# Kernel tuning notes

Measured on AMD Instinct MI355X. Metric: run time of the kernel, lower is better.

## Reference

```python
import jax, jax.numpy as jnp
import numpy as np

NUM_HEADS = 8

def setup_inputs() -> dict:
    key = jax.random.key(0)
    ks = jax.random.split(key, 10)
    B, S, D = 4, 2048, 512
    scale = 1.0 / np.sqrt(D)
    return {
        "x": jax.random.normal(ks[0], (B, S, D), dtype=jnp.float32),
        "q": jax.random.normal(ks[1], (B, S, D), dtype=jnp.float32),
        "Wq": jax.random.normal(ks[2], (D, D), dtype=jnp.float32) * scale,
        "bq": jax.random.normal(ks[3], (D,), dtype=jnp.float32) * 0.01,
        "Wk": jax.random.normal(ks[4], (D, D), dtype=jnp.float32) * scale,
        "bk": jax.random.normal(ks[5], (D,), dtype=jnp.float32) * 0.01,
        "Wv": jax.random.normal(ks[6], (D, D), dtype=jnp.float32) * scale,
        "bv": jax.random.normal(ks[7], (D,), dtype=jnp.float32) * 0.01,
        "Wo": jax.random.normal(ks[8], (D, D), dtype=jnp.float32) * scale,
        "bo": jax.random.normal(ks[9], (D,), dtype=jnp.float32) * 0.01,
    }

def reference(x, q, Wq, bq, Wk, bk, Wv, bv, Wo, bo):
    B, S, D = x.shape
    H = NUM_HEADS
    Dh = D // H
    # Linear layers: y = x @ W.T + b (torch nn.Linear convention)
    def split_heads(t):  # [B,S,D] -> [B,H,S,Dh]
        return t.reshape(B, -1, H, Dh).transpose(0, 2, 1, 3)
    Q = split_heads(q @ Wq.T + bq)
    K = split_heads(x @ Wk.T + bk)
    V = split_heads(x @ Wv.T + bv)
    logits = jnp.einsum('bhqd,bhkd->bhqk', Q, K) / jnp.sqrt(jnp.asarray(Dh, Q.dtype))
    attn = jax.nn.softmax(logits, axis=-1)
    out = jnp.einsum('bhqk,bhkd->bhqd', attn, V)  # [B,H,S,Dh]
    concat = out.transpose(0, 2, 1, 3).reshape(B, -1, D)
    return concat @ Wo.T + bo
```

## Files before the change

kernel.cpp:

```cpp
#include <hip/hip_runtime.h>
#include <stdint.h>

typedef __bf16 bf16_t;
typedef bf16_t bf16x8 __attribute__((ext_vector_type(8)));
typedef bf16_t bf16x4 __attribute__((ext_vector_type(4)));
typedef bf16_t bf16x2 __attribute__((ext_vector_type(2)));
typedef float f32x4 __attribute__((ext_vector_type(4)));
typedef float f32x16 __attribute__((ext_vector_type(16)));
typedef uint32_t u32x4 __attribute__((ext_vector_type(4)));

#define DEV __device__ __forceinline__

DEV void gload_lds16(const void* g, void* l) {
  __builtin_amdgcn_global_load_lds(
      (__attribute__((address_space(1))) void*)(g),
      (__attribute__((address_space(3))) void*)(l), 16, 0, 0);
}

__global__ __launch_bounds__(256) void cvt_all_kernel(
    const float* __restrict__ x, const float* __restrict__ q,
    const float* __restrict__ Wq, const float* __restrict__ Wk,
    const float* __restrict__ Wv, const float* __restrict__ Wo,
    bf16_t* __restrict__ xb, bf16_t* __restrict__ qb, bf16_t* __restrict__ Wb) {
  const int y = blockIdx.y;
  int i = blockIdx.x * 256 + threadIdx.x;
  const float* s;
  bf16_t* d;
  if (y == 0) { s = x; d = xb; }
  else if (y == 1) { s = q; d = qb; }
  else {
    if (i >= 131072) return;
    int widx = i >> 15;
    s = (widx == 0) ? Wq : (widx == 1) ? Wk : (widx == 2) ? Wv : Wo;
    d = Wb + (size_t)widx * 262144;
    i &= 32767;
  }
  const float4* sp = (const float4*)s + (size_t)i * 2;
  float4 a = sp[0], b = sp[1];
  bf16x8 o;
  o[0] = (bf16_t)a.x; o[1] = (bf16_t)a.y; o[2] = (bf16_t)a.z; o[3] = (bf16_t)a.w;
  o[4] = (bf16_t)b.x; o[5] = (bf16_t)b.y; o[6] = (bf16_t)b.z; o[7] = (bf16_t)b.w;
  *(bf16x8*)(d + (size_t)i * 8) = o;
}

DEV void gemm_core(const bf16_t* __restrict__ A, const bf16_t* __restrict__ W,
                   char* smem, f32x4 (&acc)[4][4]) {
  const int tid = threadIdx.x;
  const int lane = tid & 63;
  const int wid = tid >> 6;
  const int wr = wid >> 1, wc = wid & 1;
  const int bx = blockIdx.x, by = blockIdx.y;

  uint32_t goffA[4], goffB[4], ldsoff[4];
#pragma unroll
  for (int c = 0; c < 4; ++c) {
    uint32_t o = (uint32_t)wid * 4096u + (uint32_t)c * 1024u + (uint32_t)lane * 16u;
    uint32_t row = o >> 7;
    uint32_t inner = (o & 127u) ^ ((row & 7u) << 4);
    goffA[c] = ((uint32_t)by * 128u + row) * 1024u + inner;
    goffB[c] = ((uint32_t)bx * 128u + row) * 1024u + inner;
    ldsoff[c] = o - (uint32_t)lane * 16u;
  }
  uint32_t offA[4][2], offB[4][2];
#pragma unroll
  for (int i = 0; i < 4; ++i)
#pragma unroll
    for (int kk = 0; kk < 2; ++kk) {
      uint32_t ra = (uint32_t)(wr * 64 + i * 16 + (lane & 15));
      offA[i][kk] = ra * 128u + (((uint32_t)kk * 64u + ((lane >> 4) * 16u)) ^ ((ra & 7u) << 4));
      uint32_t rb = (uint32_t)(wc * 64 + i * 16 + (lane & 15));
      offB[i][kk] = rb * 128u + (((uint32_t)kk * 64u + ((lane >> 4) * 16u)) ^ ((rb & 7u) << 4));
    }

  const char* Ab = (const char*)A;
  const char* Wb = (const char*)W;

#pragma unroll
  for (int c = 0; c < 4; ++c) {
    gload_lds16(Ab + goffA[c], smem + ldsoff[c]);
    gload_lds16(Wb + goffB[c], smem + 16384 + ldsoff[c]);
  }
  asm volatile("s_waitcnt vmcnt(0)" ::: "memory");
  __syncthreads();

#pragma unroll 1
  for (int kt = 0; kt < 8; ++kt) {
    const int buf = kt & 1;
    char* cur = smem + buf * 32768;
    if (kt < 7) {
      char* nxt = smem + (buf ^ 1) * 32768;
      uint32_t gk = (uint32_t)(kt + 1) * 128u;
#pragma unroll
      for (int c = 0; c < 4; ++c) {
        gload_lds16(Ab + goffA[c] + gk, nxt + ldsoff[c]);
        gload_lds16(Wb + goffB[c] + gk, nxt + 16384 + ldsoff[c]);
      }
    }
    bf16x8 af[4][2], bfr[4][2];
#pragma unroll
    for (int kk = 0; kk < 2; ++kk)
#pragma unroll
      for (int i = 0; i < 4; ++i) {
        af[i][kk] = *(const bf16x8*)(cur + offA[i][kk]);
        bfr[i][kk] = *(const bf16x8*)(cur + 16384 + offB[i][kk]);
      }
    __builtin_amdgcn_s_setprio(1);
#pragma unroll
    for (int kk = 0; kk < 2; ++kk)
#pragma unroll
      for (int mi = 0; mi < 4; ++mi)
#pragma unroll
        for (int nj = 0; nj < 4; ++nj)
          acc[mi][nj] = __builtin_amdgcn_mfma_f32_16x16x32_bf16(
              af[mi][kk], bfr[nj][kk], acc[mi][nj], 0, 0, 0);
    __builtin_amdgcn_s_setprio(0);
    asm volatile("s_waitcnt vmcnt(0)" ::: "memory");
    __syncthreads();
  }
}

__global__ __launch_bounds__(256) void gemm_qkv_kernel(
    const bf16_t* __restrict__ xb, const bf16_t* __restrict__ qb,
    const bf16_t* __restrict__ Wb, const float* __restrict__ bq,
    const float* __restrict__ bk, const float* __restrict__ bv,
    bf16_t* __restrict__ Qh, bf16_t* __restrict__ Kh, bf16_t* __restrict__ VT) {
  __shared__ char smem[65536];
  const int z = blockIdx.z;
  const bf16_t* A = (z == 0) ? qb : xb;
  const bf16_t* W = Wb + (size_t)z * 262144;
  const float* bias = (z == 0) ? bq : (z == 1) ? bk : bv;

  f32x4 acc[4][4] = {};
  gemm_core(A, W, smem, acc);

  const int lane = threadIdx.x & 63, wid = threadIdx.x >> 6;
  const int wr = wid >> 1, wc = wid & 1;
  const int colbase = blockIdx.x * 128 + wc * 64 + (lane & 15);
  const int rowbase = blockIdx.y * 128 + wr * 64 + ((lane >> 4) << 2);

  if (z == 2) {
#pragma unroll
    for (int nj = 0; nj < 4; ++nj) {
      int c = colbase + nj * 16;
      float bb = bias[c];
      int h = c >> 6, d = c & 63;
#pragma unroll
      for (int mi = 0; mi < 4; ++mi) {
        int r0 = rowbase + mi * 16;
        int b = r0 >> 11, s0 = r0 & 2047;
        bf16x4 v;
#pragma unroll
        for (int rr = 0; rr < 4; ++rr) v[rr] = (bf16_t)(acc[mi][nj][rr] + bb);
        *(bf16x4*)(VT + ((size_t)((b << 3) | h) * 64 + d) * 2048 + s0) = v;
      }
    }
  } else {
    bf16_t* O = (z == 0) ? Qh : Kh;
    const float scl = (z == 0) ? 0.18033688f : 1.0f;
#pragma unroll
    for (int nj = 0; nj < 4; ++nj) {
      int c = colbase + nj * 16;
      float bb = bias[c];
      int h = c >> 6, d = c & 63;
#pragma unroll
      for (int mi = 0; mi < 4; ++mi)
#pragma unroll
        for (int rr = 0; rr < 4; ++rr) {
          int r = rowbase + mi * 16 + rr;
          int b = r >> 11, s = r & 2047;
          O[((size_t)((b << 3) | h) * 2048 + s) * 64 + d] = (bf16_t)((acc[mi][nj][rr] + bb) * scl);
        }
    }
  }
}

__global__ __launch_bounds__(256) void gemm_out_kernel(
    const bf16_t* __restrict__ ctx, const bf16_t* __restrict__ Wo,
    const float* __restrict__ bo, float* __restrict__ out) {
  __shared__ char smem[65536];
  f32x4 acc[4][4] = {};
  gemm_core(ctx, Wo, smem, acc);

  const int lane = threadIdx.x & 63, wid = threadIdx.x >> 6;
  const int wr = wid >> 1, wc = wid & 1;
  const int colbase = blockIdx.x * 128 + wc * 64 + (lane & 15);
  const int rowbase = blockIdx.y * 128 + wr * 64 + ((lane >> 4) << 2);
#pragma unroll
  for (int nj = 0; nj < 4; ++nj) {
    int c = colbase + nj * 16;
    float bb = bo[c];
#pragma unroll
    for (int mi = 0; mi < 4; ++mi)
#pragma unroll
      for (int rr = 0; rr < 4; ++rr) {
        int r = rowbase + mi * 16 + rr;
        out[(size_t)r * 512 + c] = acc[mi][nj][rr] + bb;
      }
  }
}

__global__ __launch_bounds__(256, 2) void attn_kernel(
    const bf16_t* __restrict__ Qh, const bf16_t* __restrict__ Kh,
    const bf16_t* __restrict__ VT, bf16_t* __restrict__ ctx) {
  __shared__ char smem[32768];
  char* Kb = smem;
  char* Vb = smem + 16384;
  const int tid = threadIdx.x, lane = tid & 63, wid = tid >> 6;
  const int l31 = lane & 31, h = lane >> 5;
  const int bid = blockIdx.x + 16 * blockIdx.y;
  const int qt = (bid >> 3) & 15;
  const int bh = (bid & 7) * 4 + (bid >> 7);

  const char* Kbase = (const char*)Kh + (size_t)bh * 262144;
  const char* Vbase = (const char*)VT + (size_t)bh * 262144;
  const char* Qbase = (const char*)Qh + (size_t)bh * 262144;

  const int qrow = qt * 128 + wid * 32 + l31;
  bf16x8 qf[4];
#pragma unroll
  for (int ks = 0; ks < 4; ++ks)
    qf[ks] = *(const bf16x8*)(Qbase + (size_t)qrow * 128 + ks * 32 + h * 16);

  uint32_t kgo[2], vgo[2], lo[2];
#pragma unroll
  for (int c = 0; c < 2; ++c) {
    uint32_t o = (uint32_t)c * 4096u + (uint32_t)wid * 1024u + (uint32_t)lane * 16u;
    uint32_t row = o >> 7;
    uint32_t inner = (o & 127u) ^ ((row & 7u) << 4);
    kgo[c] = row * 128u + inner;
    vgo[c] = row * 4096u + inner;
    lo[c] = o - (uint32_t)lane * 16u;
  }

  const uint32_t swz = (uint32_t)(l31 & 7) << 4;
  uint32_t fbase[2], fcol[4];
#pragma unroll
  for (int c = 0; c < 2; ++c) fbase[c] = (uint32_t)(32 * c + l31) * 128u;
#pragma unroll
  for (int ks = 0; ks < 4; ++ks) fcol[ks] = ((uint32_t)(ks * 32 + h * 16)) ^ swz;

  f32x16 oacc[2] = {};
  float m_run = 0.0f, l_part = 0.f;

#pragma unroll
  for (int c = 0; c < 2; ++c) {
    gload_lds16(Kbase + kgo[c], Kb + lo[c]);
    gload_lds16(Vbase + vgo[c], Vb + lo[c]);
  }
  asm volatile("s_waitcnt vmcnt(0)" ::: "memory");
  __syncthreads();

#pragma unroll 1
  for (int t = 0; t < 32; ++t) {
    const uint32_t cur = ((uint32_t)t & 1u) << 13;
    if (t < 31) {
      const uint32_t nxt = cur ^ 8192u;
      const char* Kn = Kbase + (size_t)(t + 1) * 8192;
      const char* Vn = Vbase + (size_t)(t + 1) * 128;
#pragma unroll
      for (int c = 0; c < 2; ++c) {
        gload_lds16(Kn + kgo[c], Kb + nxt + lo[c]);
        gload_lds16(Vn + vgo[c], Vb + nxt + lo[c]);
      }
    }

    f32x16 sT[2] = {};
#pragma unroll
    for (int c = 0; c < 2; ++c) {
      __builtin_amdgcn_s_setprio(1);
#pragma unroll
      for (int ks = 0; ks < 4; ++ks) {
        bf16x8 kf = *(const bf16x8*)(Kb + cur + fbase[c] + fcol[ks]);
        sT[c] = __builtin_amdgcn_mfma_f32_32x32x16_bf16(kf, qf[ks], sT[c], 0, 0, 0);
      }
      __builtin_amdgcn_s_setprio(0);
    }

    uint32_t cw[2][8];
    float la0 = 0.f, la1 = 0.f, la2 = 0.f, la3 = 0.f;
#pragma unroll
    for (int c = 0; c < 2; ++c)
#pragma unroll
      for (int w = 0; w < 8; ++w) {
        float p0 = __builtin_exp2f(sT[c][2 * w] - m_run);
        float p1 = __builtin_exp2f(sT[c][2 * w + 1] - m_run);
        if ((w & 3) == 0) la0 += p0 + p1;
        else if ((w & 3) == 1) la1 += p0 + p1;
        else if ((w & 3) == 2) la2 += p0 + p1;
        else la3 += p0 + p1;
        bf16x2 tp; tp[0] = (bf16_t)p0; tp[1] = (bf16_t)p1;
        cw[c][w] = __builtin_bit_cast(uint32_t, tp);
      }
    float ladd = (la0 + la1) + (la2 + la3);
    if (!__all(ladd <= 16384.0f)) {
      float mx = sT[0][0];
#pragma unroll
      for (int c = 0; c < 2; ++c)
#pragma unroll
        for (int r = 0; r < 16; ++r) mx = fmaxf(mx, sT[c][r]);
      mx = fmaxf(mx, __shfl_xor(mx, 32));
      float mnew = fmaxf(m_run, mx);
      float sc = __builtin_exp2f(m_run - mnew);
      l_part *= sc;
#pragma unroll
      for (int r = 0; r < 16; ++r) { oacc[0][r] *= sc; oacc[1][r] *= sc; }
      m_run = mnew;
      la0 = la1 = la2 = la3 = 0.f;
#pragma unroll
      for (int c = 0; c < 2; ++c)
#pragma unroll
        for (int w = 0; w < 8; ++w) {
          float p0 = __builtin_exp2f(sT[c][2 * w] - m_run);
          float p1 = __builtin_exp2f(sT[c][2 * w + 1] - m_run);
          if ((w & 3) == 0) la0 += p0 + p1;
          else if ((w & 3) == 1) la1 += p0 + p1;
          else if ((w & 3) == 2) la2 += p0 + p1;
          else la3 += p0 + p1;
          bf16x2 tp; tp[0] = (bf16_t)p0; tp[1] = (bf16_t)p1;
          cw[c][w] = __builtin_bit_cast(uint32_t, tp);
        }
      ladd = (la0 + la1) + (la2 + la3);
    }
    l_part += ladd;

    bf16x8 pa[4];
#pragma unroll
    for (int s = 0; s < 4; ++s) {
      const int c = s >> 1, sp = s & 1;
      uint32_t w0 = cw[c][4 * sp + 0], w1 = cw[c][4 * sp + 1];
      uint32_t w2 = cw[c][4 * sp + 2], w3 = cw[c][4 * sp + 3];
      uint32_t snd0 = h ? w0 : w2;
      uint32_t snd1 = h ? w1 : w3;
      uint32_t rcv0 = (uint32_t)__shfl_xor((int)snd0, 32);
      uint32_t rcv1 = (uint32_t)__shfl_xor((int)snd1, 32);
      u32x4 ta;
      ta[0] = h ? rcv0 : w0;
      ta[1] = h ? rcv1 : w1;
      ta[2] = h ? w2 : rcv0;
      ta[3] = h ? w3 : rcv1;
      pa[s] = __builtin_bit_cast(bf16x8, ta);
    }

#pragma unroll
    for (int dc = 0; dc < 2; ++dc) {
      __builtin_amdgcn_s_setprio(1);
#pragma unroll
      for (int ks = 0; ks < 4; ++ks) {
        bf16x8 vf = *(const bf16x8*)(Vb + cur + fbase[dc] + fcol[ks]);
        oacc[dc] = __builtin_amdgcn_mfma_f32_32x32x16_bf16(vf, pa[ks], oacc[dc], 0, 0, 0);
      }
      __builtin_amdgcn_s_setprio(0);
    }

    asm volatile("s_waitcnt vmcnt(0)" ::: "memory");
    __syncthreads();
  }

  float l = l_part + __shfl_xor(l_part, 32);
  float inv = 1.0f / l;
  const int b = bh >> 3, hh = bh & 7;
  bf16_t* crow = ctx + ((size_t)(b * 2048 + qrow)) * 512 + hh * 64;
#pragma unroll
  for (int dc = 0; dc < 2; ++dc)
#pragma unroll
    for (int m = 0; m < 4; ++m) {
      bf16x4 v;
#pragma unroll
      for (int r = 0; r < 4; ++r) v[r] = (bf16_t)(oacc[dc][4 * m + r] * inv);
      *(bf16x4*)(crow + dc * 32 + m * 8 + h * 4) = v;
    }
}

extern "C" void kernel_launch(void* const* d_in, const int* in_sizes, int n_in,
                              void* d_out, int out_size, void* d_ws, size_t ws_size,
                              hipStream_t stream) {
  const float* x  = (const float*)d_in[0];
  const float* q  = (const float*)d_in[1];
  const float* Wq = (const float*)d_in[2];
  const float* bq = (const float*)d_in[3];
  const float* Wk = (const float*)d_in[4];
  const float* bk = (const float*)d_in[5];
  const float* Wv = (const float*)d_in[6];
  const float* bv = (const float*)d_in[7];
  const float* Wo = (const float*)d_in[8];
  const float* bo = (const float*)d_in[9];

  char* ws = (char*)d_ws;
  bf16_t* xb  = (bf16_t*)(ws + 0);
  bf16_t* qb  = (bf16_t*)(ws + 8388608);
  bf16_t* Wb  = (bf16_t*)(ws + 16777216);
  bf16_t* Qh  = (bf16_t*)(ws + 18874368);
  bf16_t* Kh  = (bf16_t*)(ws + 27262976);
  bf16_t* VT  = (bf16_t*)(ws + 35651584);
  bf16_t* ctx = (bf16_t*)(ws + 44040192);

  cvt_all_kernel<<<dim3(2048, 3), 256, 0, stream>>>(x, q, Wq, Wk, Wv, Wo, xb, qb, Wb);
  gemm_qkv_kernel<<<dim3(4, 64, 3), 256, 0, stream>>>(xb, qb, Wb, bq, bk, bv, Qh, Kh, VT);
  attn_kernel<<<dim3(16, 32), 256, 0, stream>>>(Qh, Kh, VT, ctx);
  gemm_out_kernel<<<dim3(4, 64), 256, 0, stream>>>(ctx, Wb + 3 * 262144, bo, (float*)d_out);
}
```

Before: 117.3 us.

## Process two KV tiles per barrier with a four-slot LDS ring in attention

The attention kernel's LDS staging grows from a double buffer to a four-slot ring (64 KB). Each outer iteration prefetches two future K/V tiles and then computes two tiles before a single wait and barrier. This halves the number of vmcnt waits and __syncthreads and gives loads more time to land. In exchange, the doubled shared memory per block may limit residency to two blocks per CU, which matches the launch bound, and register pressure may rise from the unrolled inner pair.

Result: no change. 116.1 us (-1.1%).

```diff
diff --git a/kernel.cpp b/kernel.cpp
--- a/kernel.cpp
+++ b/kernel.cpp
@@ -202,9 +202,7 @@
 __global__ __launch_bounds__(256, 2) void attn_kernel(
     const bf16_t* __restrict__ Qh, const bf16_t* __restrict__ Kh,
     const bf16_t* __restrict__ VT, bf16_t* __restrict__ ctx) {
-  __shared__ char smem[32768];
-  char* Kb = smem;
-  char* Vb = smem + 16384;
+  __shared__ char smem[65536];
   const int tid = threadIdx.x, lane = tid & 63, wid = tid >> 6;
   const int l31 = lane & 31, h = lane >> 5;
   const int bid = blockIdx.x + 16 * blockIdx.y;
@@ -243,69 +241,56 @@
   float m_run = 0.0f, l_part = 0.f;
 
 #pragma unroll
-  for (int c = 0; c < 2; ++c) {
-    gload_lds16(Kbase + kgo[c], Kb + lo[c]);
-    gload_lds16(Vbase + vgo[c], Vb + lo[c]);
+  for (int tt = 0; tt < 2; ++tt) {
+    const char* Kt = Kbase + (size_t)tt * 8192;
+    const char* Vt = Vbase + (size_t)tt * 128;
+#pragma unroll
+    for (int c = 0; c < 2; ++c) {
+      gload_lds16(Kt + kgo[c], smem + tt * 8192 + lo[c]);
+      gload_lds16(Vt + vgo[c], smem + 32768 + tt * 8192 + lo[c]);
+    }
   }
   asm volatile("s_waitcnt vmcnt(0)" ::: "memory");
   __syncthreads();
 
 #pragma unroll 1
-  for (int t = 0; t < 32; ++t) {
-    const uint32_t cur = ((uint32_t)t & 1u) << 13;
-    if (t < 31) {
-      const uint32_t nxt = cur ^ 8192u;
-      const char* Kn = Kbase + (size_t)(t + 1) * 8192;
-      const char* Vn = Vbase + (size_t)(t + 1) * 128;
+  for (int te = 0; te < 16; ++te) {
+    const int t0 = te * 2;
+    if (t0 < 30) {
+#pragma unroll
+      for (int j = 2; j < 4; ++j) {
+        const int tn = t0 + j;
+        const uint32_t nb = ((uint32_t)tn & 3u) * 8192u;
+        const char* Kn = Kbase + (size_t)tn * 8192;
+        const char* Vn = Vbase + (size_t)tn * 128;
+#pragma unroll
+        for (int c = 0; c < 2; ++c) {
+          gload_lds16(Kn + kgo[c], smem + nb + lo[c]);
+          gload_lds16(Vn + vgo[c], smem + 32768 + nb + lo[c]);
+        }
+      }
+    }
+
+#pragma unroll
+    for (int j = 0; j < 2; ++j) {
+      const uint32_t cur = ((uint32_t)(t0 + j) & 3u) * 8192u;
+      const char* Kc = smem + cur;
+      const char* Vc = smem + 32768 + cur;
+
+      f32x16 sT[2] = {};
 #pragma unroll
       for (int c = 0; c < 2; ++c) {
-        gload_lds16(Kn + kgo[c], Kb + nxt + lo[c]);
-        gload_lds16(Vn + vgo[c], Vb + nxt + lo[c]);
-      }
-    }
-
-    f32x16 sT[2] = {};
-#pragma unroll
-    for (int c = 0; c < 2; ++c) {
-      __builtin_amdgcn_s_setprio(1);
-#pragma unroll
-      for (int ks = 0; ks < 4; ++ks) {
-        bf16x8 kf = *(const bf16x8*)(Kb + cur + fbase[c] + fcol[ks]);
-        sT[c] = __builtin_amdgcn_mfma_f32_32x32x16_bf16(kf, qf[ks], sT[c], 0, 0, 0);
-      }
-      __builtin_amdgcn_s_setprio(0);
-    }
-
-    uint32_t cw[2][8];
-    float la0 = 0.f, la1 = 0.f, la2 = 0.f, la3 = 0.f;
-#pragma unroll
-    for (int c = 0; c < 2; ++c)
-#pragma unroll
-      for (int w = 0; w < 8; ++w) {
-        float p0 = __builtin_exp2f(sT[c][2 * w] - m_run);
-        float p1 = __builtin_exp2f(sT[c][2 * w + 1] - m_run);
-        if ((w & 3) == 0) la0 += p0 + p1;
-        else if ((w & 3) == 1) la1 += p0 + p1;
-        else if ((w & 3) == 2) la2 += p0 + p1;
-        else la3 += p0 + p1;
-        bf16x2 tp; tp[0] = (bf16_t)p0; tp[1] = (bf16_t)p1;
-        cw[c][w] = __builtin_bit_cast(uint32_t, tp);
-      }
-    float ladd = (la0 + la1) + (la2 + la3);
-    if (!__all(ladd <= 16384.0f)) {
-      float mx = sT[0][0];
-#pragma unroll
-      for (int c = 0; c < 2; ++c)
-#pragma unroll
-        for (int r = 0; r < 16; ++r) mx = fmaxf(mx, sT[c][r]);
-      mx = fmaxf(mx, __shfl_xor(mx, 32));
-      float mnew = fmaxf(m_run, mx);
-      float sc = __builtin_exp2f(m_run - mnew);
-      l_part *= sc;
-#pragma unroll
-      for (int r = 0; r < 16; ++r) { oacc[0][r] *= sc; oacc[1][r] *= sc; }
-      m_run = mnew;
-      la0 = la1 = la2 = la3 = 0.f;
+        __builtin_amdgcn_s_setprio(1);
+#pragma unroll
+        for (int ks = 0; ks < 4; ++ks) {
+          bf16x8 kf = *(const bf16x8*)(Kc + fbase[c] + fcol[ks]);
+          sT[c] = __builtin_amdgcn_mfma_f32_32x32x16_bf16(kf, qf[ks], sT[c], 0, 0, 0);
+        }
+        __builtin_amdgcn_s_setprio(0);
+      }
+
+      uint32_t cw[2][8];
+      float la0 = 0.f, la1 = 0.f, la2 = 0.f, la3 = 0.f;
 #pragma unroll
       for (int c = 0; c < 2; ++c)
 #pragma unroll
@@ -319,37 +304,66 @@
           bf16x2 tp; tp[0] = (bf16_t)p0; tp[1] = (bf16_t)p1;
           cw[c][w] = __builtin_bit_cast(uint32_t, tp);
         }
-      ladd = (la0 + la1) + (la2 + la3);
-    }
-    l_part += ladd;
-
-    bf16x8 pa[4];
-#pragma unroll
-    for (int s = 0; s < 4; ++s) {
-      const int c = s >> 1, sp = s & 1;
-      uint32_t w0 = cw[c][4 * sp + 0], w1 = cw[c][4 * sp + 1];
-      uint32_t w2 = cw[c][4 * sp + 2], w3 = cw[c][4 * sp + 3];
-      uint32_t snd0 = h ? w0 : w2;
-      uint32_t snd1 = h ? w1 : w3;
-      uint32_t rcv0 = (uint32_t)__shfl_xor((int)snd0, 32);
-      uint32_t rcv1 = (uint32_t)__shfl_xor((int)snd1, 32);
-      u32x4 ta;
-      ta[0] = h ? rcv0 : w0;
-      ta[1] = h ? rcv1 : w1;
-      ta[2] = h ? w2 : rcv0;
-      ta[3] = h ? w3 : rcv1;
-      pa[s] = __builtin_bit_cast(bf16x8, ta);
-    }
-
-#pragma unroll
-    for (int dc = 0; dc < 2; ++dc) {
-      __builtin_amdgcn_s_setprio(1);
-#pragma unroll
-      for (int ks = 0; ks < 4; ++ks) {
-        bf16x8 vf = *(const bf16x8*)(Vb + cur + fbase[dc] + fcol[ks]);
-        oacc[dc] = __builtin_amdgcn_mfma_f32_32x32x16_bf16(vf, pa[ks], oacc[dc], 0, 0, 0);
-      }
-      __builtin_amdgcn_s_setprio(0);
+      float ladd = (la0 + la1) + (la2 + la3);
+      if (!__all(ladd <= 16384.0f)) {
+        float mx = sT[0][0];
+#pragma unroll
+        for (int c = 0; c < 2; ++c)
+#pragma unroll
+          for (int r = 0; r < 16; ++r) mx = fmaxf(mx, sT[c][r]);
+        mx = fmaxf(mx, __shfl_xor(mx, 32));
+        float mnew = fmaxf(m_run, mx);
+        float sc = __builtin_exp2f(m_run - mnew);
+        l_part *= sc;
+#pragma unroll
+        for (int r = 0; r < 16; ++r) { oacc[0][r] *= sc; oacc[1][r] *= sc; }
+        m_run = mnew;
+        la0 = la1 = la2 = la3 = 0.f;
+#pragma unroll
+        for (int c = 0; c < 2; ++c)
+#pragma unroll
+          for (int w = 0; w < 8; ++w) {
+            float p0 = __builtin_exp2f(sT[c][2 * w] - m_run);
+            float p1 = __builtin_exp2f(sT[c][2 * w + 1] - m_run);
+            if ((w & 3) == 0) la0 += p0 + p1;
+            else if ((w & 3) == 1) la1 += p0 + p1;
+            else if ((w & 3) == 2) la2 += p0 + p1;
+            else la3 += p0 + p1;
+            bf16x2 tp; tp[0] = (bf16_t)p0; tp[1] = (bf16_t)p1;
+            cw[c][w] = __builtin_bit_cast(uint32_t, tp);
+          }
+        ladd = (la0 + la1) + (la2 + la3);
+      }
+      l_part += ladd;
+
+      bf16x8 pa[4];
+#pragma unroll
+      for (int s = 0; s < 4; ++s) {
+        const int c = s >> 1, sp = s & 1;
+        uint32_t w0 = cw[c][4 * sp + 0], w1 = cw[c][4 * sp + 1];
+        uint32_t w2 = cw[c][4 * sp + 2], w3 = cw[c][4 * sp + 3];
+        uint32_t snd0 = h ? w0 : w2;
+        uint32_t snd1 = h ? w1 : w3;
+        uint32_t rcv0 = (uint32_t)__shfl_xor((int)snd0, 32);
+        uint32_t rcv1 = (uint32_t)__shfl_xor((int)snd1, 32);
+        u32x4 ta;
+        ta[0] = h ? rcv0 : w0;
+        ta[1] = h ? rcv1 : w1;
+        ta[2] = h ? w2 : rcv0;
+        ta[3] = h ? w3 : rcv1;
+        pa[s] = __builtin_bit_cast(bf16x8, ta);
+      }
+
+#pragma unroll
+      for (int dc = 0; dc < 2; ++dc) {
+        __builtin_amdgcn_s_setprio(1);
+#pragma unroll
+        for (int ks = 0; ks < 4; ++ks) {
+          bf16x8 vf = *(const bf16x8*)(Vc + fbase[dc] + fcol[ks]);
+          oacc[dc] = __builtin_amdgcn_mfma_f32_32x32x16_bf16(vf, pa[ks], oacc[dc], 0, 0, 0);
+        }
+        __builtin_amdgcn_s_setprio(0);
+      }
     }
 
     asm volatile("s_waitcnt vmcnt(0)" ::: "memory");
```
